# Kernel tuning notes

Hardware: AMD Instinct MI355X
Metric: run time of the kernel (lower is better)

## Reference

```python
import jax, jax.numpy as jnp
import numpy as np

DIM = 1024
HEADS = 16
HEAD_DIM = DIM // HEADS
WINDOW = 512
NEG = -1e9  # matches masked_fill(-1e9) semantics; excluded keys get ~0 weight


def setup_inputs() -> dict:
    key = jax.random.key(0)
    ks = jax.random.split(key, 9)
    s = 1.0 / np.sqrt(DIM)
    inp = {"x": jax.random.normal(ks[0], (2, 4096, DIM), dtype=jnp.float32)}
    for i, name in enumerate(["q", "k", "v", "o"]):
        inp[f"W{name}"] = jax.random.uniform(ks[1 + 2 * i], (DIM, DIM), jnp.float32, -s, s)
        inp[f"b{name}"] = jax.random.uniform(ks[2 + 2 * i], (DIM,), jnp.float32, -s, s)
    return inp


def _sliding_window_attn(x, Wq, bq, Wk, bk, Wv, bv, Wo, bo):
    B, S, D = x.shape
    H, hd, W = HEADS, HEAD_DIM, WINDOW
    nb = S // W  # number of query blocks

    def proj(Wp, bp):
        y = x @ Wp.T + bp                       # [B,S,D]
        return y.reshape(B, S, H, hd).transpose(0, 2, 1, 3)  # [B,H,S,hd]

    q = proj(Wq, bq)
    k = proj(Wk, bk)
    v = proj(Wv, bv)

    scale = hd ** -0.5
    qb = q.reshape(B, H, nb, W, hd)

    def window_kv(t):
        # each query block n attends to blocks n-1 and n (2W keys)
        pad = jnp.concatenate([jnp.zeros((B, H, W, hd), t.dtype), t], axis=2)
        prev = pad[:, :, :S].reshape(B, H, nb, W, hd)
        cur = t.reshape(B, H, nb, W, hd)
        return jnp.concatenate([prev, cur], axis=3)  # [B,H,nb,2W,hd]

    kw = window_kv(k)
    vw = window_kv(v)

    scores = jnp.einsum('bhnqd,bhnkd->bhnqk', qb, kw) * scale  # [B,H,nb,W,2W]

    # key abs pos = n*W - W + t ; query abs pos = n*W + s
    t = jnp.arange(2 * W)            # [2W]
    s_ = jnp.arange(W)[:, None]      # [W,1]
    n = jnp.arange(nb)[:, None, None]  # [nb,1,1]
    valid = (t <= s_ + W) & (t >= s_ + 1) & (n * W - W + t >= 0)  # [nb,W,2W]
    scores = jnp.where(valid, scores, NEG)

    attn = jax.nn.softmax(scores, axis=-1)
    out = jnp.einsum('bhnqk,bhnkd->bhnqd', attn, vw)  # [B,H,nb,W,hd]
    out = out.reshape(B, H, S, hd).transpose(0, 2, 1, 3).reshape(B, S, D)
    return out @ Wo.T + bo


def reference(x, Wq, bq, Wk, bk, Wv, bv, Wo, bo):
    return _sliding_window_attn(x, Wq, bq, Wk, bk, Wv, bv, Wo, bo)
```

## Files before the change

kernel.cpp:

```cpp
#include <hip/hip_runtime.h>
#include <hip/hip_bf16.h>

typedef __bf16 bf16_t;
typedef __attribute__((ext_vector_type(8))) __bf16 bfrag;
typedef __attribute__((ext_vector_type(4))) __bf16 bf16x4;
typedef __attribute__((ext_vector_type(4))) float f32x4;

#define SEQ    4096
#define NDIM   1024
#define NHEAD  16
#define HD     64
#define NBATCH 2
#define MROWS  (NBATCH * SEQ)
#define LQK    2048
#define PSTR   76

__device__ __forceinline__ void gload_lds16(const bf16_t* g, bf16_t* l) {
    __builtin_amdgcn_global_load_lds(
        (const __attribute__((address_space(1))) unsigned int*)g,
        (__attribute__((address_space(3))) unsigned int*)l,
        16, 0, 0);
}

__device__ __forceinline__ void block_sync() {
    asm volatile("" ::: "memory");
    __builtin_amdgcn_s_barrier();
    asm volatile("" ::: "memory");
}

__device__ __forceinline__ void stage_half(const bf16_t* __restrict__ G, int ldg,
                                           int grow0, int gk0, bf16_t* region,
                                           int half, int tid)
{
    const int poff = half * 8192 + tid * 16;
    const int loff = poff ^ (((poff >> 9) & 1) << 5);
    const int r    = loff >> 6;
    const int cb   = loff & 63;
    const bf16_t* src = G + (size_t)(grow0 + r) * ldg + gk0 + (cb >> 1);
    gload_lds16(src, region + ((half * 8192 + (tid >> 6) * 1024) >> 1));
}

__device__ __forceinline__ bfrag ldsfrag(const bf16_t* region, int R, int quad)
{
    const int off = (R * 64 + quad * 16) ^ (((R >> 3) & 1) << 5);
    return *(const bfrag*)((const char*)region + off);
}

__global__ __launch_bounds__(512, 2)
void gemm256(const bf16_t* __restrict__ A, int lda,
             const bf16_t* __restrict__ W,
             const float* __restrict__ b0p, const float* __restrict__ b1p,
             const float* __restrict__ b2p, float qscale,
             bf16_t* __restrict__ C, int ldc, int K,
             bf16_t* __restrict__ VtOut)
{
    __shared__ __align__(1024) bf16_t LSD[32768];

    const int tid  = threadIdx.x;
    const int lane = tid & 63;
    const int n16  = lane & 15;
    const int quad = lane >> 4;
    const int wm   = (tid >> 6) >> 2;
    const int wn   = (tid >> 6) & 3;
    const int row0 = blockIdx.y * 256;
    const int col0 = blockIdx.x * 256;
    const int nt   = K >> 5;

    f32x4 acc[8][4];
#pragma unroll
    for (int m = 0; m < 8; m++)
#pragma unroll
        for (int j = 0; j < 4; j++) acc[m][j] = (f32x4){0.f, 0.f, 0.f, 0.f};

    {
        bf16_t* A0 = &LSD[0];
        bf16_t* B0 = &LSD[8192];
        bf16_t* B1 = &LSD[16384 + 8192];
        stage_half(A, lda, row0, 0, A0, 0, tid);
        stage_half(A, lda, row0, 0, A0, 1, tid);
        stage_half(W, K, col0, 0, B0, 0, tid);
        stage_half(W, K, col0, 0, B0, 1, tid);
        stage_half(W, K, col0, 32, B1, 0, tid);
        stage_half(W, K, col0, 32, B1, 1, tid);
    }
    asm volatile("s_waitcnt vmcnt(2)" ::: "memory");

    for (int t = 0; t < nt; ++t) {
        bf16_t* Ab  = &LSD[(t & 1) * 16384];
        bf16_t* Bb  = Ab + 8192;
        bf16_t* AbN = &LSD[((t & 1) ^ 1) * 16384];

        bfrag a[4], b[4];

        block_sync();
#pragma unroll
        for (int m = 0; m < 4; m++) a[m] = ldsfrag(Ab, wm * 128 + m * 16 + n16, quad);
#pragma unroll
        for (int j = 0; j < 4; j++) b[j] = ldsfrag(Bb, wn * 64 + j * 16 + n16, quad);
        if (t + 1 < nt) {
            stage_half(A, lda, row0, (t + 1) * 32, AbN, 0, tid);
            stage_half(A, lda, row0, (t + 1) * 32, AbN, 1, tid);
        }
        asm volatile("s_waitcnt lgkmcnt(0)" ::: "memory");
        __builtin_amdgcn_sched_barrier(0);
        __builtin_amdgcn_s_setprio(1);
#pragma unroll
        for (int m = 0; m < 4; m++)
#pragma unroll
            for (int j = 0; j < 4; j++)
                acc[m][j] = __builtin_amdgcn_mfma_f32_16x16x32_bf16(a[m], b[j], acc[m][j], 0, 0, 0);
        __builtin_amdgcn_s_setprio(0);

        block_sync();
#pragma unroll
        for (int m = 0; m < 4; m++) a[m] = ldsfrag(Ab, wm * 128 + (m + 4) * 16 + n16, quad);
        if (t + 2 < nt) {
            stage_half(W, K, col0, (t + 2) * 32, Bb, 0, tid);
            stage_half(W, K, col0, (t + 2) * 32, Bb, 1, tid);
        }
        asm volatile("s_waitcnt lgkmcnt(0)" ::: "memory");
        __builtin_amdgcn_sched_barrier(0);
        __builtin_amdgcn_s_setprio(1);
#pragma unroll
        for (int m = 0; m < 4; m++)
#pragma unroll
            for (int j = 0; j < 4; j++)
                acc[m + 4][j] = __builtin_amdgcn_mfma_f32_16x16x32_bf16(a[m], b[j], acc[m + 4][j], 0, 0, 0);
        __builtin_amdgcn_s_setprio(0);

        if (t < nt - 2) asm volatile("s_waitcnt vmcnt(2)" ::: "memory");
        else            asm volatile("s_waitcnt vmcnt(0)" ::: "memory");
    }

    const float* bias = (col0 < 1024) ? b0p : (col0 < 2048 ? b1p : b2p);
    const float bsc   = (col0 < 1024) ? qscale : 1.0f;
    const int bcol0   = col0 & 1023;

    if (col0 < 2048 || VtOut == nullptr) {
#pragma unroll
        for (int m = 0; m < 8; m++)
#pragma unroll
            for (int j = 0; j < 4; j++)
#pragma unroll
                for (int r = 0; r < 4; r++) {
                    int row = row0 + wm * 128 + m * 16 + quad * 4 + r;
                    int col = wn * 64 + j * 16 + n16;
                    float v = acc[m][j][r] + bias[bcol0 + col] * bsc;
                    C[(size_t)row * ldc + col0 + col] = (bf16_t)v;
                }
    } else {
#pragma unroll
        for (int m = 0; m < 8; m++) {
#pragma unroll
            for (int j = 0; j < 4; j++) {
                int dg     = col0 + wn * 64 + j * 16 + n16 - 2048;
                int token0 = row0 + wm * 128 + m * 16 + quad * 4;
                int bb     = token0 >> 12;
                float bv   = bias[bcol0 + wn * 64 + j * 16 + n16];
                size_t vrow = ((size_t)bb * NHEAD + (dg >> 6)) * HD + (dg & 63);
                bf16x4 pk;
#pragma unroll
                for (int r = 0; r < 4; r++) pk[r] = (__bf16)(acc[m][j][r] + bv);
                *(bf16x4*)&VtOut[vrow * SEQ + (token0 & (SEQ - 1))] = pk;
            }
        }
    }
}

template <typename OT>
__global__ __launch_bounds__(256, 2)
void gemm_bt(const bf16_t* __restrict__ A, int lda,
             const bf16_t* __restrict__ W,
             const float* __restrict__ b0p, const float* __restrict__ b1p,
             const float* __restrict__ b2p, float qscale,
             OT* __restrict__ C, int ldc, int K,
             bf16_t* __restrict__ VtOut)
{
    __shared__ __align__(16) bf16_t As[128 * 32];
    __shared__ __align__(16) bf16_t Bs[128 * 32];

    const int tid  = threadIdx.x;
    const int lane = tid & 63;
    const int wid  = tid >> 6;
    const int n16  = lane & 15;
    const int quad = lane >> 4;
    const int row0 = blockIdx.y * 128;
    const int col0 = blockIdx.x * 128;
    const int wrow = (wid >> 1) * 64;
    const int wcol = (wid & 1) * 64;
    const float* bias = (col0 < 1024) ? b0p : (col0 < 2048 ? b1p : b2p);
    const float bsc = (col0 < 1024) ? qscale : 1.0f;
    const int bcol0 = col0 & 1023;

    f32x4 acc[4][4];
#pragma unroll
    for (int i = 0; i < 4; i++)
#pragma unroll
        for (int j = 0; j < 4; j++) acc[i][j] = (f32x4){0.f, 0.f, 0.f, 0.f};

    for (int k0 = 0; k0 < K; k0 += 32) {
#pragma unroll
        for (int it = 0; it < 2; it++) {
            int idx = tid + it * 256;
            int r   = idx >> 2;
            int c   = (idx & 3) * 8;
            gload_lds16(A + (size_t)(row0 + r) * lda + k0 + c, &As[(it * 256 + wid * 64) * 8]);
            gload_lds16(W + (size_t)(col0 + r) * K   + k0 + c, &Bs[(it * 256 + wid * 64) * 8]);
        }
        __syncthreads();

        bfrag af[4], bfg[4];
#pragma unroll
        for (int i = 0; i < 4; i++)
            af[i] = *(const bfrag*)(&As[(wrow + i * 16 + n16) * 32 + quad * 8]);
#pragma unroll
        for (int j = 0; j < 4; j++)
            bfg[j] = *(const bfrag*)(&Bs[(wcol + j * 16 + n16) * 32 + quad * 8]);

#pragma unroll
        for (int i = 0; i < 4; i++)
#pragma unroll
            for (int j = 0; j < 4; j++)
                acc[i][j] = __builtin_amdgcn_mfma_f32_16x16x32_bf16(af[i], bfg[j], acc[i][j], 0, 0, 0);
        __syncthreads();
    }

    if (col0 < 2048 || VtOut == nullptr) {
#pragma unroll
        for (int i = 0; i < 4; i++)
#pragma unroll
            for (int j = 0; j < 4; j++)
#pragma unroll
                for (int r = 0; r < 4; r++) {
                    int row = row0 + wrow + i * 16 + quad * 4 + r;
                    int col = wcol + j * 16 + n16;
                    float v = acc[i][j][r] + bias[bcol0 + col] * bsc;
                    C[(size_t)row * ldc + col0 + col] = (OT)v;
                }
    } else {
#pragma unroll
        for (int i = 0; i < 4; i++) {
#pragma unroll
            for (int j = 0; j < 4; j++) {
                int dg     = col0 + wcol + j * 16 + n16 - 2048;
                int token0 = row0 + wrow + i * 16 + quad * 4;
                int bb     = token0 >> 12;
                float bv   = bias[bcol0 + wcol + j * 16 + n16];
                size_t vrow = ((size_t)bb * NHEAD + (dg >> 6)) * HD + (dg & 63);
                bf16x4 pk;
#pragma unroll
                for (int r = 0; r < 4; r++) pk[r] = (__bf16)(acc[i][j][r] + bv);
                *(bf16x4*)&VtOut[vrow * SEQ + (token0 & (SEQ - 1))] = pk;
            }
        }
    }
}

__global__ __launch_bounds__(256)
void cast_x(const float* __restrict__ s, bf16_t* __restrict__ d)
{
    size_t i = ((size_t)blockIdx.x * 256 + threadIdx.x) * 8;
    float4 a = *(const float4*)(s + i);
    float4 b = *(const float4*)(s + i + 4);
    bfrag o;
    o[0] = (__bf16)a.x; o[1] = (__bf16)a.y; o[2] = (__bf16)a.z; o[3] = (__bf16)a.w;
    o[4] = (__bf16)b.x; o[5] = (__bf16)b.y; o[6] = (__bf16)b.z; o[7] = (__bf16)b.w;
    *(bfrag*)(d + i) = o;
}

__global__ __launch_bounds__(256)
void cast_w(const float* __restrict__ wq, const float* __restrict__ wk,
            const float* __restrict__ wv, const float* __restrict__ wo,
            bf16_t* __restrict__ d)
{
    size_t t   = (size_t)blockIdx.x * 256 + threadIdx.x;
    int    sel = (int)(t >> 17);
    const float* s = sel == 0 ? wq : (sel == 1 ? wk : (sel == 2 ? wv : wo));
    const float sc = (sel == 0) ? 0.125f : 1.0f;
    size_t off = (t & 131071) * 8;
    float4 a = *(const float4*)(s + off);
    float4 b = *(const float4*)(s + off + 4);
    bfrag o;
    o[0] = (__bf16)(a.x * sc); o[1] = (__bf16)(a.y * sc);
    o[2] = (__bf16)(a.z * sc); o[3] = (__bf16)(a.w * sc);
    o[4] = (__bf16)(b.x * sc); o[5] = (__bf16)(b.y * sc);
    o[6] = (__bf16)(b.z * sc); o[7] = (__bf16)(b.w * sc);
    *(bfrag*)(d + (size_t)sel * 1048576 + off) = o;
}

__global__ __launch_bounds__(256, 4)
void attn_win(const bf16_t* __restrict__ QK, const bf16_t* __restrict__ Vt,
              bf16_t* __restrict__ AO)
{
    __shared__ __align__(16) bf16_t Ks[2][64 * 72];
    __shared__ __align__(16) bf16_t Pw[4][32 * PSTR];

    const int tid  = threadIdx.x;
    const int wid  = tid >> 6;
    const int lane = tid & 63;
    const int n16  = lane & 15;
    const int quad = lane >> 4;

    const int lin = blockIdx.x;
    const int sub = lin >> 3;
    const int bh  = (lin & 7) * 4 + (sub >> 5);
    const int qt  = sub & 31;
    const int qb0 = qt * 128;

    const int b  = bh >> 4, h = bh & 15;
    const size_t bS   = (size_t)b * SEQ;
    const size_t hoff = (size_t)h * HD;
    const bf16_t* Vb  = Vt + (size_t)bh * HD * SEQ;
    const int wstart  = qb0 - 512;
    const int it0     = (qb0 < 512) ? ((512 - qb0) >> 6) : 0;

    const int srow  = tid >> 2;
    const int scol0 = (tid & 3) * 16;

    const int qwmin = qb0 + wid * 32;
    const int qwmax = qwmin + 31;
    int qa[2];
    bfrag bq0[2], bq1[2];
#pragma unroll
    for (int qg = 0; qg < 2; qg++) {
        qa[qg] = qwmin + qg * 16 + n16;
        bq0[qg] = *(const bfrag*)(&QK[(bS + qa[qg]) * LQK + hoff + quad * 8]);
        bq1[qg] = *(const bfrag*)(&QK[(bS + qa[qg]) * LQK + hoff + 32 + quad * 8]);
    }

    f32x4 ao[2][4];
#pragma unroll
    for (int qg = 0; qg < 2; qg++)
#pragma unroll
        for (int j = 0; j < 4; j++) ao[qg][j] = (f32x4){0.f, 0.f, 0.f, 0.f};
    float m[2] = {-1e30f, -1e30f}, l[2] = {0.f, 0.f};

    uint4 kp0, kp1;
    {
        const bf16_t* src = &QK[(bS + wstart + it0 * 64 + srow) * LQK + 1024 + hoff + scol0];
        kp0 = *(const uint4*)(src);
        kp1 = *(const uint4*)(src + 8);
    }

    for (int it = it0; it < 10; ++it) {
        const int k0 = wstart + it * 64;
        const int pb = it & 1;
        *(uint4*)(&Ks[pb][srow * 72 + scol0])     = kp0;
        *(uint4*)(&Ks[pb][srow * 72 + scol0 + 8]) = kp1;
        __syncthreads();
        if (it < 9) {
            const bf16_t* src = &QK[(bS + wstart + (it + 1) * 64 + srow) * LQK + 1024 + hoff + scol0];
            kp0 = *(const uint4*)(src);
            kp1 = *(const uint4*)(src + 8);
        }

        if (k0 > qwmax || k0 + 63 < qwmin - 511) continue;

        f32x4 a[2][4];
#pragma unroll
        for (int nt = 0; nt < 4; nt++) {
            bfrag ak0 = *(const bfrag*)(&Ks[pb][(nt * 16 + n16) * 72 + quad * 8]);
            bfrag ak1 = *(const bfrag*)(&Ks[pb][(nt * 16 + n16) * 72 + 32 + quad * 8]);
#pragma unroll
            for (int qg = 0; qg < 2; qg++) {
                f32x4 s4 = (f32x4){0.f, 0.f, 0.f, 0.f};
                s4 = __builtin_amdgcn_mfma_f32_16x16x32_bf16(ak0, bq0[qg], s4, 0, 0, 0);
                s4 = __builtin_amdgcn_mfma_f32_16x16x32_bf16(ak1, bq1[qg], s4, 0, 0, 0);
                a[qg][nt] = s4;
            }
        }

#pragma unroll
        for (int qg = 0; qg < 2; qg++) {
            const int gmin = qwmin + qg * 16, gmax = gmin + 15;
            const bool msk = !((k0 >= gmax - 511) & (k0 + 63 <= gmin));
            if (msk) {
#pragma unroll
                for (int nt = 0; nt < 4; nt++)
#pragma unroll
                    for (int r = 0; r < 4; r++) {
                        int ka = k0 + nt * 16 + quad * 4 + r;
                        bool valid = (ka >= qa[qg] - 511) & (ka <= qa[qg]);
                        if (!valid) a[qg][nt][r] = -1e30f;
                    }
            }

            float cm = -1e30f;
#pragma unroll
            for (int nt = 0; nt < 4; nt++)
#pragma unroll
                for (int r = 0; r < 4; r++) cm = fmaxf(cm, a[qg][nt][r]);
            cm = fmaxf(cm, __shfl_xor(cm, 16, 64));
            cm = fmaxf(cm, __shfl_xor(cm, 32, 64));
            float mn    = fmaxf(m[qg], cm);
            float alpha = __expf(m[qg] - mn);
            m[qg] = mn;
#pragma unroll
            for (int j = 0; j < 4; j++)
#pragma unroll
                for (int r = 0; r < 4; r++) ao[qg][j][r] *= alpha;

            float lacc = 0.f;
#pragma unroll
            for (int nt = 0; nt < 4; nt++) {
                bf16x4 pk;
#pragma unroll
                for (int r = 0; r < 4; r++) {
                    float p = __expf(a[qg][nt][r] - m[qg]);
                    lacc += p;
                    pk[r] = (__bf16)p;
                }
                *(bf16x4*)&Pw[wid][(qg * 16 + n16) * PSTR + nt * 16 + quad * 4] = pk;
            }
            l[qg] = l[qg] * alpha + lacc;
        }

#pragma unroll
        for (int ks = 0; ks < 2; ks++) {
            bfrag bp[2];
#pragma unroll
            for (int qg = 0; qg < 2; qg++)
                bp[qg] = *(const bfrag*)(&Pw[wid][(qg * 16 + n16) * PSTR + ks * 32 + quad * 8]);
#pragma unroll
            for (int j = 0; j < 4; j++) {
                bfrag av = *(const bfrag*)(&Vb[(size_t)(j * 16 + n16) * SEQ
                                               + k0 + ks * 32 + quad * 8]);
#pragma unroll
                for (int qg = 0; qg < 2; qg++)
                    ao[qg][j] = __builtin_amdgcn_mfma_f32_16x16x32_bf16(av, bp[qg], ao[qg][j], 0, 0, 0);
            }
        }
    }

#pragma unroll
    for (int qg = 0; qg < 2; qg++) {
        float lv = l[qg];
        lv += __shfl_xor(lv, 16, 64);
        lv += __shfl_xor(lv, 32, 64);
        const float inv = 1.0f / lv;
#pragma unroll
        for (int j = 0; j < 4; j++) {
            bf16x4 pk;
#pragma unroll
            for (int r = 0; r < 4; r++) pk[r] = (__bf16)(ao[qg][j][r] * inv);
            *(bf16x4*)&AO[(bS + qa[qg]) * NDIM + hoff + j * 16 + quad * 4] = pk;
        }
    }
}

extern "C" void kernel_launch(void* const* d_in, const int* in_sizes, int n_in,
                              void* d_out, int out_size, void* d_ws, size_t ws_size,
                              hipStream_t stream)
{
    const float* x  = (const float*)d_in[0];
    const float* Wq = (const float*)d_in[1];
    const float* bq = (const float*)d_in[2];
    const float* Wk = (const float*)d_in[3];
    const float* bk = (const float*)d_in[4];
    const float* Wv = (const float*)d_in[5];
    const float* bv = (const float*)d_in[6];
    const float* Wo = (const float*)d_in[7];
    const float* bo = (const float*)d_in[8];
    float* out = (float*)d_out;

    const size_t QK_E = (size_t)MROWS * LQK;
    const size_t X_E  = (size_t)MROWS * NDIM;
    if (ws_size < (QK_E + X_E + 4u * 1048576u) * sizeof(bf16_t)) return;

    bf16_t* QKb = (bf16_t*)d_ws;
    bf16_t* AbX = QKb + QK_E;
    bf16_t* Wc  = AbX + X_E;
    bf16_t* Wob = Wc + 3u * 1048576u;
    bf16_t* Vtg = (bf16_t*)d_out;

    dim3 blk(256);

    cast_x<<<dim3(4096), blk, 0, stream>>>(x, AbX);
    cast_w<<<dim3(2048), blk, 0, stream>>>(Wq, Wk, Wv, Wo, Wc);

    gemm256<<<dim3(3072 / 256, MROWS / 256), dim3(512), 0, stream>>>(
        AbX, NDIM, Wc, bq, bk, bv, 0.125f, QKb, LQK, NDIM, Vtg);

    attn_win<<<dim3(1024), dim3(256), 0, stream>>>(QKb, Vtg, AbX);

    gemm_bt<float><<<dim3(NDIM / 128, MROWS / 128), blk, 0, stream>>>(
        AbX, NDIM, Wob, bo, bo, bo, 1.0f, out, NDIM, NDIM, nullptr);
}
```

Before: 269.9 us.

## Deepen QKV GEMM pipeline to 4-slot LDS ring with dynamic 128KB shared memory

New measurement: 274.4 us. No clear change (+1.7%).

```diff
diff --git a/kernel.cpp b/kernel.cpp
--- a/kernel.cpp
+++ b/kernel.cpp
@@ -22,29 +22,11 @@
         16, 0, 0);
 }
 
-__device__ __forceinline__ void block_sync() {
-    asm volatile("" ::: "memory");
-    __builtin_amdgcn_s_barrier();
-    asm volatile("" ::: "memory");
-}
-
-__device__ __forceinline__ void stage_half(const bf16_t* __restrict__ G, int ldg,
-                                           int grow0, int gk0, bf16_t* region,
-                                           int half, int tid)
-{
-    const int poff = half * 8192 + tid * 16;
-    const int loff = poff ^ (((poff >> 9) & 1) << 5);
-    const int r    = loff >> 6;
-    const int cb   = loff & 63;
-    const bf16_t* src = G + (size_t)(grow0 + r) * ldg + gk0 + (cb >> 1);
-    gload_lds16(src, region + ((half * 8192 + (tid >> 6) * 1024) >> 1));
-}
-
-__device__ __forceinline__ bfrag ldsfrag(const bf16_t* region, int R, int quad)
-{
-    const int off = (R * 64 + quad * 16) ^ (((R >> 3) & 1) << 5);
-    return *(const bfrag*)((const char*)region + off);
-}
+#define BAR()  do { asm volatile("" ::: "memory"); __builtin_amdgcn_s_barrier(); \
+                    asm volatile("" ::: "memory"); } while (0)
+#define LGKM0() do { asm volatile("s_waitcnt lgkmcnt(0)" ::: "memory"); \
+                     __builtin_amdgcn_sched_barrier(0); } while (0)
+#define VMC(n)  asm volatile("s_waitcnt vmcnt(" #n ")" ::: "memory")
 
 __global__ __launch_bounds__(512, 2)
 void gemm256(const bf16_t* __restrict__ A, int lda,
@@ -54,17 +36,31 @@
              bf16_t* __restrict__ C, int ldc, int K,
              bf16_t* __restrict__ VtOut)
 {
-    __shared__ __align__(1024) bf16_t LSD[32768];
+    extern __shared__ bf16_t LDS[];
 
     const int tid  = threadIdx.x;
     const int lane = tid & 63;
     const int n16  = lane & 15;
     const int quad = lane >> 4;
-    const int wm   = (tid >> 6) >> 2;
-    const int wn   = (tid >> 6) & 3;
+    const int wid  = tid >> 6;
+    const int wm   = wid >> 2;
+    const int wn   = wid & 3;
     const int row0 = blockIdx.y * 256;
     const int col0 = blockIdx.x * 256;
-    const int nt   = K >> 5;
+    const int NT   = K >> 6;
+
+    int poff0 = tid * 16;
+    int loff0 = poff0 ^ (((poff0 >> 9) & 1) << 5);
+    int poff1 = 8192 + tid * 16;
+    int loff1 = poff1 ^ (((poff1 >> 9) & 1) << 5);
+    const int r0 = loff0 >> 6, c0 = (loff0 & 63) >> 1;
+    const int r1 = loff1 >> 6, c1 = (loff1 & 63) >> 1;
+    const bf16_t* Asrc0 = A + (size_t)(row0 + r0) * lda + c0;
+    const bf16_t* Asrc1 = A + (size_t)(row0 + r1) * lda + c1;
+    const bf16_t* Wsrc0 = W + (size_t)(col0 + r0) * K + c0;
+    const bf16_t* Wsrc1 = W + (size_t)(col0 + r1) * K + c1;
+    bf16_t* const dst0 = LDS;
+    const int wb = wid * 512;
 
     f32x4 acc[8][4];
 #pragma unroll
@@ -72,65 +68,132 @@
 #pragma unroll
         for (int j = 0; j < 4; j++) acc[m][j] = (f32x4){0.f, 0.f, 0.f, 0.f};
 
-    {
-        bf16_t* A0 = &LSD[0];
-        bf16_t* B0 = &LSD[8192];
-        bf16_t* B1 = &LSD[16384 + 8192];
-        stage_half(A, lda, row0, 0, A0, 0, tid);
-        stage_half(A, lda, row0, 0, A0, 1, tid);
-        stage_half(W, K, col0, 0, B0, 0, tid);
-        stage_half(W, K, col0, 0, B0, 1, tid);
-        stage_half(W, K, col0, 32, B1, 0, tid);
-        stage_half(W, K, col0, 32, B1, 1, tid);
-    }
-    asm volatile("s_waitcnt vmcnt(2)" ::: "memory");
-
-    for (int t = 0; t < nt; ++t) {
-        bf16_t* Ab  = &LSD[(t & 1) * 16384];
-        bf16_t* Bb  = Ab + 8192;
-        bf16_t* AbN = &LSD[((t & 1) ^ 1) * 16384];
-
-        bfrag a[4], b[4];
-
-        block_sync();
-#pragma unroll
-        for (int m = 0; m < 4; m++) a[m] = ldsfrag(Ab, wm * 128 + m * 16 + n16, quad);
-#pragma unroll
-        for (int j = 0; j < 4; j++) b[j] = ldsfrag(Bb, wn * 64 + j * 16 + n16, quad);
-        if (t + 1 < nt) {
-            stage_half(A, lda, row0, (t + 1) * 32, AbN, 0, tid);
-            stage_half(A, lda, row0, (t + 1) * 32, AbN, 1, tid);
-        }
-        asm volatile("s_waitcnt lgkmcnt(0)" ::: "memory");
-        __builtin_amdgcn_sched_barrier(0);
+#define SLOT(d, op, h) ((d) * 32768 + (op) * 16384 + (h) * 8192)
+#define STAGE(srcA0, srcA1, slot, gk)                                   \
+    do { gload_lds16((srcA0) + (gk), dst0 + (slot) + wb);               \
+         gload_lds16((srcA1) + (gk), dst0 + (slot) + 4096 + wb); } while (0)
+
+    STAGE(Wsrc0, Wsrc1, SLOT(0,1,0), 0);
+    STAGE(Asrc0, Asrc1, SLOT(0,0,0), 0);
+    STAGE(Wsrc0, Wsrc1, SLOT(0,1,1), 32);
+    STAGE(Asrc0, Asrc1, SLOT(0,0,1), 32);
+    STAGE(Wsrc0, Wsrc1, SLOT(1,1,0), 64);
+    STAGE(Asrc0, Asrc1, SLOT(1,0,0), 64);
+    STAGE(Wsrc0, Wsrc1, SLOT(1,1,1), 96);
+    VMC(10);
+    BAR();
+
+    for (int s = 0; s < NT; ++s) {
+        const int d = s & 1;
+        bfrag af[4], bf[4];
+
+        {
+            const bf16_t* sA = LDS + SLOT(d, 0, 0);
+            const bf16_t* sB = LDS + SLOT(d, 1, 0);
+#pragma unroll
+            for (int f = 0; f < 4; f++) {
+                int off = ((wm * 128 + f * 16 + n16) << 6) + (quad << 4);
+                off ^= ((off >> 9) & 1) << 5;
+                af[f] = *(const bfrag*)((const char*)sA + off);
+            }
+#pragma unroll
+            for (int j = 0; j < 4; j++) {
+                int off = ((wn * 64 + j * 16 + n16) << 6) + (quad << 4);
+                off ^= ((off >> 9) & 1) << 5;
+                bf[j] = *(const bfrag*)((const char*)sB + off);
+            }
+        }
+        if (s + 1 < NT) STAGE(Asrc0, Asrc1, SLOT(d ^ 1, 0, 1), (s + 1) * 64 + 32);
+        BAR();
+        LGKM0();
         __builtin_amdgcn_s_setprio(1);
 #pragma unroll
-        for (int m = 0; m < 4; m++)
-#pragma unroll
-            for (int j = 0; j < 4; j++)
-                acc[m][j] = __builtin_amdgcn_mfma_f32_16x16x32_bf16(a[m], b[j], acc[m][j], 0, 0, 0);
+        for (int f = 0; f < 4; f++)
+#pragma unroll
+            for (int j = 0; j < 4; j++)
+                acc[f][j] = __builtin_amdgcn_mfma_f32_16x16x32_bf16(af[f], bf[j], acc[f][j], 0, 0, 0);
         __builtin_amdgcn_s_setprio(0);
-
-        block_sync();
-#pragma unroll
-        for (int m = 0; m < 4; m++) a[m] = ldsfrag(Ab, wm * 128 + (m + 4) * 16 + n16, quad);
-        if (t + 2 < nt) {
-            stage_half(W, K, col0, (t + 2) * 32, Bb, 0, tid);
-            stage_half(W, K, col0, (t + 2) * 32, Bb, 1, tid);
-        }
-        asm volatile("s_waitcnt lgkmcnt(0)" ::: "memory");
-        __builtin_amdgcn_sched_barrier(0);
+        BAR();
+
+        {
+            const bf16_t* sA = LDS + SLOT(d, 0, 0);
+#pragma unroll
+            for (int f = 0; f < 4; f++) {
+                int off = ((wm * 128 + (f + 4) * 16 + n16) << 6) + (quad << 4);
+                off ^= ((off >> 9) & 1) << 5;
+                af[f] = *(const bfrag*)((const char*)sA + off);
+            }
+        }
+        if (s + 2 < NT) STAGE(Wsrc0, Wsrc1, SLOT(d, 1, 0), (s + 2) * 64);
+        BAR();
+        LGKM0();
         __builtin_amdgcn_s_setprio(1);
 #pragma unroll
-        for (int m = 0; m < 4; m++)
-#pragma unroll
-            for (int j = 0; j < 4; j++)
-                acc[m + 4][j] = __builtin_amdgcn_mfma_f32_16x16x32_bf16(a[m], b[j], acc[m + 4][j], 0, 0, 0);
+        for (int f = 0; f < 4; f++)
+#pragma unroll
+            for (int j = 0; j < 4; j++)
+                acc[f + 4][j] = __builtin_amdgcn_mfma_f32_16x16x32_bf16(af[f], bf[j], acc[f + 4][j], 0, 0, 0);
         __builtin_amdgcn_s_setprio(0);
-
-        if (t < nt - 2) asm volatile("s_waitcnt vmcnt(2)" ::: "memory");
-        else            asm volatile("s_waitcnt vmcnt(0)" ::: "memory");
-    }
+        if (s < NT - 2)       VMC(10);
+        else if (s == NT - 2) VMC(8);
+        else                  VMC(0);
+        BAR();
+
+        {
+            const bf16_t* sA = LDS + SLOT(d, 0, 1);
+            const bf16_t* sB = LDS + SLOT(d, 1, 1);
+#pragma unroll
+            for (int f = 0; f < 4; f++) {
+                int off = ((wm * 128 + f * 16 + n16) << 6) + (quad << 4);
+                off ^= ((off >> 9) & 1) << 5;
+                af[f] = *(const bfrag*)((const char*)sA + off);
+            }
+#pragma unroll
+            for (int j = 0; j < 4; j++) {
+                int off = ((wn * 64 + j * 16 + n16) << 6) + (quad << 4);
+                off ^= ((off >> 9) & 1) << 5;
+                bf[j] = *(const bfrag*)((const char*)sB + off);
+            }
+        }
+        if (s + 2 < NT) STAGE(Asrc0, Asrc1, SLOT(d, 0, 0), (s + 2) * 64);
+        BAR();
+        LGKM0();
+        __builtin_amdgcn_s_setprio(1);
+#pragma unroll
+        for (int f = 0; f < 4; f++)
+#pragma unroll
+            for (int j = 0; j < 4; j++)
+                acc[f][j] = __builtin_amdgcn_mfma_f32_16x16x32_bf16(af[f], bf[j], acc[f][j], 0, 0, 0);
+        __builtin_amdgcn_s_setprio(0);
+        BAR();
+
+        {
+            const bf16_t* sA = LDS + SLOT(d, 0, 1);
+#pragma unroll
+            for (int f = 0; f < 4; f++) {
+                int off = ((wm * 128 + (f + 4) * 16 + n16) << 6) + (quad << 4);
+                off ^= ((off >> 9) & 1) << 5;
+                af[f] = *(const bfrag*)((const char*)sA + off);
+            }
+        }
+        if (s + 2 < NT) STAGE(Wsrc0, Wsrc1, SLOT(d, 1, 1), (s + 2) * 64 + 32);
+        BAR();
+        LGKM0();
+        __builtin_amdgcn_s_setprio(1);
+#pragma unroll
+        for (int f = 0; f < 4; f++)
+#pragma unroll
+            for (int j = 0; j < 4; j++)
+                acc[f + 4][j] = __builtin_amdgcn_mfma_f32_16x16x32_bf16(af[f], bf[j], acc[f + 4][j], 0, 0, 0);
+        __builtin_amdgcn_s_setprio(0);
+        if (s + 1 < NT) {
+            if (s < NT - 2) VMC(10);
+            else            VMC(4);
+        }
+        BAR();
+    }
+#undef STAGE
+#undef SLOT
 
     const float* bias = (col0 < 1024) ? b0p : (col0 < 2048 ? b1p : b2p);
     const float bsc   = (col0 < 1024) ? qscale : 1.0f;
@@ -473,13 +536,23 @@
     bf16_t* Wob = Wc + 3u * 1048576u;
     bf16_t* Vtg = (bf16_t*)d_out;
 
+    static int lds_ok = -1;
+    if (lds_ok < 0)
+        lds_ok = (hipFuncSetAttribute((const void*)gemm256,
+                   hipFuncAttributeMaxDynamicSharedMemorySize, 131072) == hipSuccess) ? 1 : 0;
+
     dim3 blk(256);
 
     cast_x<<<dim3(4096), blk, 0, stream>>>(x, AbX);
     cast_w<<<dim3(2048), blk, 0, stream>>>(Wq, Wk, Wv, Wo, Wc);
 
-    gemm256<<<dim3(3072 / 256, MROWS / 256), dim3(512), 0, stream>>>(
-        AbX, NDIM, Wc, bq, bk, bv, 0.125f, QKb, LQK, NDIM, Vtg);
+    if (lds_ok) {
+        gemm256<<<dim3(3072 / 256, MROWS / 256), dim3(512), 131072, stream>>>(
+            AbX, NDIM, Wc, bq, bk, bv, 0.125f, QKb, LQK, NDIM, Vtg);
+    } else {
+        gemm_bt<bf16_t><<<dim3(3072 / 128, MROWS / 128), blk, 0, stream>>>(
+            AbX, NDIM, Wc, bq, bk, bv, 0.125f, QKb, LQK, NDIM, Vtg);
+    }
 
     attn_win<<<dim3(1024), dim3(256), 0, stream>>>(QKb, Vtg, AbX);
 
```
